# Kernel optimization log

Measured on AMD Instinct MI355X. Metric: run time of the kernel, lower is better.

## Reference

```python
import jax, jax.numpy as jnp
import numpy as np

N_NODES = 200000
IN_DIM = 128
HID = 64
WALK_LEN = 16          # max_step + 1
NUM_WALKS = 16         # = hidden_graphs, walks per graph
N_GRAPHS = 1024
PEN = 32
N_CLASSES = 10
BN_EPS = 1e-5


def setup_inputs() -> dict:
    key = jax.random.key(0)
    ks = jax.random.split(key, 16)
    x = jax.random.normal(ks[0], (N_NODES, IN_DIM), dtype=jnp.float32)
    walks = jax.random.randint(ks[1], (N_GRAPHS * NUM_WALKS, WALK_LEN), 0, N_NODES)
    # each graph contributes NUM_WALKS consecutive walks
    walk_batch = jnp.repeat(jnp.arange(N_GRAPHS), NUM_WALKS)
    s = 1.0 / np.sqrt(HID)
    return {
        "x": x,
        "walks": walks,
        "walk_batch": walk_batch,
        "W_enc": jax.random.normal(ks[2], (HID, IN_DIM), jnp.float32) / np.sqrt(IN_DIM),
        "b_enc": jnp.zeros((HID,), jnp.float32),
        "W_ih": jax.random.uniform(ks[3], (3 * HID, HID), jnp.float32, -s, s),
        "W_hh": jax.random.uniform(ks[4], (3 * HID, HID), jnp.float32, -s, s),
        "b_ih": jax.random.uniform(ks[5], (3 * HID,), jnp.float32, -s, s),
        "b_hh": jax.random.uniform(ks[6], (3 * HID,), jnp.float32, -s, s),
        "gamma": jnp.ones((HID,), jnp.float32),
        "beta": jnp.zeros((HID,), jnp.float32),
        "W1": jax.random.normal(ks[7], (PEN, HID), jnp.float32) / np.sqrt(HID),
        "b1": jnp.zeros((PEN,), jnp.float32),
        "W2": jax.random.normal(ks[8], (N_CLASSES, PEN), jnp.float32) / np.sqrt(PEN),
        "b2": jnp.zeros((N_CLASSES,), jnp.float32),
    }


def _gru_cell(h, xt, W_ih, W_hh, b_ih, b_hh):
    # PyTorch GRU gate math
    gi = xt @ W_ih.T + b_ih            # [W, 3H]
    gh = h @ W_hh.T + b_hh             # [W, 3H]
    i_r, i_z, i_n = jnp.split(gi, 3, axis=-1)
    h_r, h_z, h_n = jnp.split(gh, 3, axis=-1)
    r = jax.nn.sigmoid(i_r + h_r)
    z = jax.nn.sigmoid(i_z + h_z)
    n = jnp.tanh(i_n + r * h_n)
    return (1.0 - z) * n + z * h


def reference(x, walks, walk_batch, W_enc, b_enc, W_ih, W_hh, b_ih, b_hh,
              gamma, beta, W1, b1, W2, b2):
    # feature encoder on all nodes, then gather along walks
    x_enc = x @ W_enc.T + b_enc                     # [N, H]
    walk_feats = x_enc[walks]                       # [W, L, H] gather
    xs = jnp.swapaxes(walk_feats, 0, 1)             # [L, W, H]

    def step(h, xt):
        return _gru_cell(h, xt, W_ih, W_hh, b_ih, b_hh), None

    h0 = jnp.zeros((walks.shape[0], HID), walk_feats.dtype)
    h_final, _ = jax.lax.scan(step, h0, xs)         # [W, H] last hidden state

    # segment-mean pooling per graph
    seg_sum = jax.ops.segment_sum(h_final, walk_batch, num_segments=N_GRAPHS)
    cnt = jax.ops.segment_sum(jnp.ones((walks.shape[0],), h_final.dtype),
                              walk_batch, num_segments=N_GRAPHS)
    graph_enc = seg_sum / jnp.maximum(cnt, 1.0)[:, None]   # [B, H]

    # BatchNorm1d (training mode: batch statistics, biased variance)
    mean = jnp.mean(graph_enc, axis=0)
    var = jnp.mean(jnp.square(graph_enc - mean), axis=0)
    gn = (graph_enc - mean) / jnp.sqrt(var + BN_EPS) * gamma + beta

    h1 = jax.nn.relu(gn @ W1.T + b1)                # dropout p=0 -> identity
    logits = h1 @ W2.T + b2
    return jax.nn.log_softmax(logits, axis=1)
```

## Files before the change

### kernel.cpp

```cpp
#include <hip/hip_runtime.h>
#include <stdint.h>

typedef _Float16 half8 __attribute__((ext_vector_type(8)));
typedef _Float16 half4 __attribute__((ext_vector_type(4)));
typedef float f32x4 __attribute__((ext_vector_type(4)));

#define MFMA_F16(A, B, C) __builtin_amdgcn_mfma_f32_16x16x32_f16(A, B, C, 0, 0, 0)

#define NN 200000
#define NT 3125
#define GSTRIDE 512

__device__ __forceinline__ void gload_lds16(const void* gp, void* lp) {
  __builtin_amdgcn_global_load_lds(
      (const __attribute__((address_space(1))) uint32_t*)(gp),
      (__attribute__((address_space(3))) uint32_t*)(lp), 16, 0, 0);
}

__global__ __launch_bounds__(256, 2) void k_enc(const float* __restrict__ x,
                                                const float* __restrict__ Wenc,
                                                const float* __restrict__ benc,
                                                _Float16* __restrict__ xenc) {
  __shared__ float xl[2][64 * 128];
  __shared__ _Float16 wlds[16 * 64 * 8];

  const int tid = threadIdx.x;
  const int lane = tid & 63, wv = tid >> 6;
  const int r = lane & 15, g = lane >> 4;
  const int t0 = blockIdx.x;

#define ISSUE8(TT, BUF)                                                        \
  {                                                                            \
    _Pragma("unroll") for (int i = 0; i < 8; ++i) {                            \
      int row = wv * 16 + 2 * i + (lane >> 5);                                 \
      int grow = (TT) * 64 + row;                                              \
      if (grow >= NN) grow = NN - 1;                                           \
      int scol = ((lane & 31) * 16) ^ ((row & 7) << 4);                        \
      gload_lds16((const char*)(x + (size_t)grow * 128) + scol,                \
                  (char*)&xl[BUF][0] + (wv * 16 + 2 * i) * 512);               \
    }                                                                          \
  }

  ISSUE8(t0, 0);
  for (int i4 = tid; i4 < 2048; i4 += 256) {
    int idx = i4 * 4;
    f32x4 v = *(const f32x4*)(Wenc + idx);
    int j = idx >> 7, k = idx & 127;
    int tile = (j >> 4) * 4 + (k >> 5);
    int ln = ((k >> 3) & 3) * 16 + (j & 15);
    half4 h;
    h[0] = (_Float16)v[0]; h[1] = (_Float16)v[1];
    h[2] = (_Float16)v[2]; h[3] = (_Float16)v[3];
    *(half4*)&wlds[(tile * 64 + ln) * 8 + (k & 7)] = h;
  }
  __syncthreads();

  half8 W[4][4];
#pragma unroll
  for (int jt = 0; jt < 4; ++jt)
#pragma unroll
    for (int kt = 0; kt < 4; ++kt)
      W[jt][kt] = *(const half8*)&wlds[((jt * 4 + kt) * 64 + lane) * 8];

  float bb[4][4];
#pragma unroll
  for (int jt = 0; jt < 4; ++jt)
#pragma unroll
    for (int rr = 0; rr < 4; ++rr) bb[jt][rr] = benc[jt * 16 + g * 4 + rr];

  const int sw = (r & 7) << 4;
  int buf = 0;

  for (int t = t0; t < NT; t += GSTRIDE) {
    int tn = t + GSTRIDE;
    if (tn < NT) {
      ISSUE8(tn, buf ^ 1);
      asm volatile("s_waitcnt vmcnt(8)" ::: "memory");
    } else {
      asm volatile("s_waitcnt vmcnt(0)" ::: "memory");
    }
    __builtin_amdgcn_sched_barrier(0);

    const char* rp = (const char*)&xl[buf][0] + (wv * 16 + r) * 512;
    f32x4 acc[4];
#pragma unroll
    for (int jt = 0; jt < 4; ++jt)
      acc[jt] = (f32x4){bb[jt][0], bb[jt][1], bb[jt][2], bb[jt][3]};

#pragma unroll
    for (int kt = 0; kt < 4; ++kt) {
      f32x4 v0 = *(const f32x4*)(rp + ((kt * 128 + g * 32) ^ sw));
      f32x4 v1 = *(const f32x4*)(rp + ((kt * 128 + g * 32 + 16) ^ sw));
      half8 a;
#pragma unroll
      for (int e = 0; e < 4; ++e) {
        a[e] = (_Float16)v0[e];
        a[4 + e] = (_Float16)v1[e];
      }
#pragma unroll
      for (int jt = 0; jt < 4; ++jt)
        acc[jt] = MFMA_F16(W[jt][kt], a, acc[jt]);
    }

    int node = t * 64 + wv * 16 + r;
    if (node < NN) {
#pragma unroll
      for (int jt = 0; jt < 4; ++jt) {
        half4 o;
        o[0] = (_Float16)acc[jt][0]; o[1] = (_Float16)acc[jt][1];
        o[2] = (_Float16)acc[jt][2]; o[3] = (_Float16)acc[jt][3];
        *(half4*)&xenc[(size_t)node * 64 + jt * 16 + g * 4] = o;
      }
    }
    buf ^= 1;
  }
#undef ISSUE8
}

__global__ __launch_bounds__(512, 4) void k_gru(const _Float16* __restrict__ xenc,
                                                const int* __restrict__ walks,
                                                const float* __restrict__ Wih,
                                                const float* __restrict__ Whh,
                                                const float* __restrict__ bih,
                                                const float* __restrict__ bhh,
                                                float* __restrict__ genc) {
  __shared__ _Float16 wih_lds[24 * 64 * 8];
  __shared__ _Float16 whh_lds[24 * 64 * 8];
  __shared__ _Float16 h_lds[2][2][16 * 64];
  __shared__ int ids[2][256];

  const int tid = threadIdx.x;
  const int lane = tid & 63, wv = tid >> 6;
  const int r = lane & 15, g = lane >> 4;
  const int p = wv & 3;
  const int gl = wv >> 2;
  const int gph = blockIdx.x * 2 + gl;

  for (int idx = tid; idx < 192 * 64; idx += 512) {
    int j = idx >> 6, k = idx & 63;
    int tile = (j >> 4) * 2 + (k >> 5);
    int ln = ((k >> 3) & 3) * 16 + (j & 15);
    int off = (tile * 64 + ln) * 8 + (k & 7);
    wih_lds[off] = (_Float16)Wih[idx];
    whh_lds[off] = (_Float16)Whh[idx];
  }

  if ((wv & 3) == 0) {
    const int* wp = walks + gph * 256;
    int4 v = *(const int4*)(wp + lane * 4);
    int vals[4] = {v.x, v.y, v.z, v.w};
#pragma unroll
    for (int i = 0; i < 4; ++i) {
      int m = lane * 4 + i;
      ids[gl][(m & 15) * 16 + (m >> 4)] = vals[i];
    }
  }

  for (int i = tid; i < 4096; i += 512) ((_Float16*)h_lds)[i] = (_Float16)0.f;

  __syncthreads();

  half8 Bi[3][2], Bh[3][2];
#pragma unroll
  for (int G = 0; G < 3; ++G)
#pragma unroll
    for (int kt = 0; kt < 2; ++kt) {
      int T = G * 4 + p;
      Bi[G][kt] = *(const half8*)&wih_lds[((T * 2 + kt) * 64 + lane) * 8];
      Bh[G][kt] = *(const half8*)&whh_lds[((T * 2 + kt) * 64 + lane) * 8];
    }

  const int j0 = p * 16 + r;
  const float br_ = bih[j0] + bhh[j0];
  const float bz_ = bih[64 + j0] + bhh[64 + j0];
  const float bin_ = bih[128 + j0];
  const float bhn_ = bhh[128 + j0];

  f32x4 h = (f32x4){0.f, 0.f, 0.f, 0.f};
  const int swz = (r & 7) << 4;

  half8 AxA0, AxA1, AxB0, AxB1;
  {
    int n0 = ids[gl][0 * 16 + r];
    const _Float16* p0 = xenc + (size_t)n0 * 64 + g * 8;
    AxA0 = *(const half8*)p0;
    AxA1 = *(const half8*)(p0 + 32);
    int n1 = ids[gl][1 * 16 + r];
    const _Float16* p1 = xenc + (size_t)n1 * 64 + g * 8;
    AxB0 = *(const half8*)p1;
    AxB1 = *(const half8*)(p1 + 32);
  }

#define GRU_STEP(T_, RB, AX0, AX1)                                             \
  {                                                                            \
    int nid = ids[gl][(((T_) + 2) & 15) * 16 + r];                             \
    const _Float16* xp = xenc + (size_t)nid * 64 + g * 8;                      \
    half8 NX0 = *(const half8*)xp;                                             \
    half8 NX1 = *(const half8*)(xp + 32);                                      \
    char* rbase = (char*)&h_lds[gl][RB][0];                                    \
    char* wbase = (char*)&h_lds[gl][RB ^ 1][0];                                \
    half8 Ah0 = *(const half8*)(rbase + ((r * 128 + g * 16) ^ swz));           \
    half8 Ah1 = *(const half8*)(rbase + ((r * 128 + 64 + g * 16) ^ swz));      \
    f32x4 aR = (f32x4){br_, br_, br_, br_};                                    \
    f32x4 aZ = (f32x4){bz_, bz_, bz_, bz_};                                    \
    f32x4 aN = (f32x4){bin_, bin_, bin_, bin_};                                \
    f32x4 aH = (f32x4){bhn_, bhn_, bhn_, bhn_};                                \
    aR = MFMA_F16(AX0, Bi[0][0], aR);                                          \
    aR = MFMA_F16(AX1, Bi[0][1], aR);                                          \
    aZ = MFMA_F16(AX0, Bi[1][0], aZ);                                          \
    aZ = MFMA_F16(AX1, Bi[1][1], aZ);                                          \
    aN = MFMA_F16(AX0, Bi[2][0], aN);                                          \
    aN = MFMA_F16(AX1, Bi[2][1], aN);                                          \
    aR = MFMA_F16(Ah0, Bh[0][0], aR);                                          \
    aR = MFMA_F16(Ah1, Bh[0][1], aR);                                          \
    aZ = MFMA_F16(Ah0, Bh[1][0], aZ);                                          \
    aZ = MFMA_F16(Ah1, Bh[1][1], aZ);                                          \
    aH = MFMA_F16(Ah0, Bh[2][0], aH);                                          \
    aH = MFMA_F16(Ah1, Bh[2][1], aH);                                          \
    _Pragma("unroll") for (int rr = 0; rr < 4; ++rr) {                         \
      float rg = __builtin_amdgcn_rcpf(1.f + __expf(-aR[rr]));                 \
      float zg = __builtin_amdgcn_rcpf(1.f + __expf(-aZ[rr]));                 \
      float pn = aN[rr] + rg * aH[rr];                                         \
      float e2 = __expf(2.f * pn);                                             \
      float nn = 1.f - 2.f * __builtin_amdgcn_rcpf(e2 + 1.f);                  \
      h[rr] = (1.f - zg) * nn + zg * h[rr];                                    \
    }                                                                          \
    if ((T_) < 15) {                                                           \
      _Pragma("unroll") for (int rr = 0; rr < 4; ++rr) {                       \
        int row = g * 4 + rr;                                                  \
        int byte = (row * 128 + j0 * 2) ^ ((row & 7) << 4);                    \
        *(_Float16*)(wbase + byte) = (_Float16)h[rr];                          \
      }                                                                        \
    }                                                                          \
    asm volatile("s_waitcnt lgkmcnt(0)" ::: "memory");                         \
    __builtin_amdgcn_s_barrier();                                              \
    __builtin_amdgcn_sched_barrier(0);                                         \
    AX0 = NX0;                                                                 \
    AX1 = NX1;                                                                 \
  }

  for (int t = 0; t < 16; t += 2) {
    GRU_STEP(t, 0, AxA0, AxA1);
    GRU_STEP(t + 1, 1, AxB0, AxB1);
  }
#undef GRU_STEP

  {
    float s = h[0] + h[1] + h[2] + h[3];
    s += __shfl_xor(s, 16);
    s += __shfl_xor(s, 32);
    if (g == 0) genc[gph * 64 + j0] = s * 0.0625f;
  }
}

__global__ __launch_bounds__(256) void k_post(const float* __restrict__ genc,
                                              const float* __restrict__ gamma,
                                              const float* __restrict__ beta,
                                              const float* __restrict__ W1,
                                              const float* __restrict__ b1,
                                              const float* __restrict__ W2,
                                              const float* __restrict__ b2,
                                              float* __restrict__ out) {
  __shared__ float sum_s[4][64], sq_s[4][64], sc[64], sh[64];
  __shared__ float w1[32 * 64], w2[10 * 32], bb1[32], bb2[10];
  const int tid = threadIdx.x;
  const int j = tid & 63, grp = tid >> 6;

  float s = 0.f, q = 0.f;
  for (int rr = 0; rr < 256; ++rr) {
    float v = genc[(grp * 256 + rr) * 64 + j];
    s += v;
    q += v * v;
  }
  sum_s[grp][j] = s;
  sq_s[grp][j] = q;

  for (int i = tid; i < 32 * 64; i += 256) w1[i] = W1[i];
  for (int i = tid; i < 10 * 32; i += 256) w2[i] = W2[i];
  if (tid < 32) bb1[tid] = b1[tid];
  if (tid >= 32 && tid < 42) bb2[tid - 32] = b2[tid - 32];
  __syncthreads();

  if (grp == 0) {
    float S = sum_s[0][j] + sum_s[1][j] + sum_s[2][j] + sum_s[3][j];
    float Q = sq_s[0][j] + sq_s[1][j] + sq_s[2][j] + sq_s[3][j];
    float mean = S * (1.f / 1024.f);
    float var = Q * (1.f / 1024.f) - mean * mean;
    float rstd = rsqrtf(var + 1e-5f);
    float scv = gamma[j] * rstd;
    sc[j] = scv;
    sh[j] = beta[j] - mean * scv;
  }
  __syncthreads();

  const int row = blockIdx.x * 256 + tid;
  float gn[64];
  const f32x4* gp = (const f32x4*)(genc + row * 64);
#pragma unroll
  for (int jq = 0; jq < 16; ++jq) {
    f32x4 v = gp[jq];
#pragma unroll
    for (int e = 0; e < 4; ++e) gn[jq * 4 + e] = v[e] * sc[jq * 4 + e] + sh[jq * 4 + e];
  }

  float h1[32];
#pragma unroll
  for (int i = 0; i < 32; ++i) {
    float a = bb1[i];
#pragma unroll
    for (int jj = 0; jj < 64; ++jj) a += w1[i * 64 + jj] * gn[jj];
    h1[i] = fmaxf(a, 0.f);
  }

  float lg[10];
  float mx = -1e30f;
#pragma unroll
  for (int c = 0; c < 10; ++c) {
    float a = bb2[c];
#pragma unroll
    for (int i = 0; i < 32; ++i) a += w2[c * 32 + i] * h1[i];
    lg[c] = a;
    mx = fmaxf(mx, a);
  }
  float se = 0.f;
#pragma unroll
  for (int c = 0; c < 10; ++c) se += __expf(lg[c] - mx);
  float lse = mx + __logf(se);
#pragma unroll
  for (int c = 0; c < 10; ++c) out[row * 10 + c] = lg[c] - lse;
}

extern "C" void kernel_launch(void* const* d_in, const int* in_sizes, int n_in,
                              void* d_out, int out_size, void* d_ws, size_t ws_size,
                              hipStream_t stream) {
  const float* x = (const float*)d_in[0];
  const int* walks = (const int*)d_in[1];
  const float* Wenc = (const float*)d_in[3];
  const float* benc = (const float*)d_in[4];
  const float* Wih = (const float*)d_in[5];
  const float* Whh = (const float*)d_in[6];
  const float* bih = (const float*)d_in[7];
  const float* bhh = (const float*)d_in[8];
  const float* gamma = (const float*)d_in[9];
  const float* beta = (const float*)d_in[10];
  const float* W1 = (const float*)d_in[11];
  const float* b1 = (const float*)d_in[12];
  const float* W2 = (const float*)d_in[13];
  const float* b2 = (const float*)d_in[14];
  float* out = (float*)d_out;

  char* ws = (char*)d_ws;
  _Float16* xenc = (_Float16*)ws;
  float* genc = (float*)(ws + 25600000);

  k_enc<<<dim3(GSTRIDE), dim3(256), 0, stream>>>(x, Wenc, benc, xenc);
  k_gru<<<dim3(512), dim3(512), 0, stream>>>(xenc, walks, Wih, Whh, bih, bhh, genc);
  k_post<<<dim3(4), dim3(256), 0, stream>>>(genc, gamma, beta, W1, b1, W2, b2, out);
}
```

Before: 81.64 us.

## Fold encoder into GRU input weights and gather raw node features per walk

Drops the full-graph encoder pass. A small prep kernel precomputes W_ih·W_enc (and the combined bias), so the GRU kernel gathers raw 128-dim fp32 rows of x only for the walked nodes. It converts them to fp16 and stages them in LDS with double buffering. This avoids encoding all 200k nodes and writing/reading the intermediate, and only 262k gathered rows are touched. In exchange the GRU does twice the input-gate MFMAs and gathers larger fp32 rows on its critical path.

```diff
diff --git a/kernel.cpp b/kernel.cpp
--- a/kernel.cpp
+++ b/kernel.cpp
@@ -2,147 +2,89 @@
 #include <stdint.h>
 
 typedef _Float16 half8 __attribute__((ext_vector_type(8)));
-typedef _Float16 half4 __attribute__((ext_vector_type(4)));
 typedef float f32x4 __attribute__((ext_vector_type(4)));
 
 #define MFMA_F16(A, B, C) __builtin_amdgcn_mfma_f32_16x16x32_f16(A, B, C, 0, 0, 0)
 
-#define NN 200000
-#define NT 3125
-#define GSTRIDE 512
-
-__device__ __forceinline__ void gload_lds16(const void* gp, void* lp) {
-  __builtin_amdgcn_global_load_lds(
-      (const __attribute__((address_space(1))) uint32_t*)(gp),
-      (__attribute__((address_space(3))) uint32_t*)(lp), 16, 0, 0);
+
+__global__ __launch_bounds__(256) void k_prep(const float* __restrict__ Wenc,
+                                              const float* __restrict__ benc,
+                                              const float* __restrict__ Wih,
+                                              const float* __restrict__ Whh,
+                                              const float* __restrict__ bih,
+                                              _Float16* __restrict__ wgi,
+                                              _Float16* __restrict__ whhp,
+                                              float* __restrict__ bc) {
+  __shared__ float wenc_s[64 * 68];
+  __shared__ float wih_s[16 * 64];
+  const int t = threadIdx.x;
+  const int bt = blockIdx.x;
+  const int jt = bt >> 1, kh = (bt & 1) << 6;
+
+  for (int i = t; i < 4096; i += 256)
+    wenc_s[(i >> 6) * 68 + (i & 63)] = Wenc[(i >> 6) * 128 + kh + (i & 63)];
+  for (int i = t; i < 1024; i += 256)
+    wih_s[i] = Wih[(jt * 16 + (i >> 6)) * 64 + (i & 63)];
+  __syncthreads();
+
+  const int jl = t >> 4, kb = (t & 15) * 4;
+  f32x4 acc = (f32x4){0.f, 0.f, 0.f, 0.f};
+  for (int m = 0; m < 64; ++m) {
+    float w = wih_s[jl * 64 + m];
+    f32x4 v = *(const f32x4*)&wenc_s[m * 68 + kb];
+    acc[0] += w * v[0]; acc[1] += w * v[1];
+    acc[2] += w * v[2]; acc[3] += w * v[3];
+  }
+#pragma unroll
+  for (int i = 0; i < 4; ++i) {
+    int k = kh + kb + i;
+    wgi[((jt * 4 + (k >> 5)) * 64 + ((k >> 3) & 3) * 16 + jl) * 8 + (k & 7)] =
+        (_Float16)acc[i];
+  }
+
+  if ((bt & 1) == 0) {
+#pragma unroll
+    for (int i = 0; i < 4; ++i) {
+      int idx = t * 4 + i;
+      int j = jt * 16 + (idx >> 6), k = idx & 63;
+      whhp[((jt * 2 + (k >> 5)) * 64 + ((k >> 3) & 3) * 16 + (j & 15)) * 8 + (k & 7)] =
+          (_Float16)Whh[j * 64 + k];
+    }
+    if (t < 16) {
+      int j = jt * 16 + t;
+      float s = bih[j];
+      for (int m = 0; m < 64; ++m) s += wih_s[t * 64 + m] * benc[m];
+      bc[j] = s;
+    }
+  }
 }
 
-__global__ __launch_bounds__(256, 2) void k_enc(const float* __restrict__ x,
-                                                const float* __restrict__ Wenc,
-                                                const float* __restrict__ benc,
-                                                _Float16* __restrict__ xenc) {
-  __shared__ float xl[2][64 * 128];
-  __shared__ _Float16 wlds[16 * 64 * 8];
+__global__ __launch_bounds__(512, 4) void k_gru(const float* __restrict__ x,
+                                                const int* __restrict__ walks,
+                                                const _Float16* __restrict__ wgi,
+                                                const _Float16* __restrict__ whhp,
+                                                const float* __restrict__ bc,
+                                                const float* __restrict__ bhh,
+                                                float* __restrict__ genc) {
+  __shared__ _Float16 xs[2][2][2048];
+  __shared__ _Float16 h_lds[2][2][1024];
+  __shared__ int ids[2][256];
 
   const int tid = threadIdx.x;
   const int lane = tid & 63, wv = tid >> 6;
   const int r = lane & 15, g = lane >> 4;
-  const int t0 = blockIdx.x;
-
-#define ISSUE8(TT, BUF)                                                        \
-  {                                                                            \
-    _Pragma("unroll") for (int i = 0; i < 8; ++i) {                            \
-      int row = wv * 16 + 2 * i + (lane >> 5);                                 \
-      int grow = (TT) * 64 + row;                                              \
-      if (grow >= NN) grow = NN - 1;                                           \
-      int scol = ((lane & 31) * 16) ^ ((row & 7) << 4);                        \
-      gload_lds16((const char*)(x + (size_t)grow * 128) + scol,                \
-                  (char*)&xl[BUF][0] + (wv * 16 + 2 * i) * 512);               \
-    }                                                                          \
-  }
-
-  ISSUE8(t0, 0);
-  for (int i4 = tid; i4 < 2048; i4 += 256) {
-    int idx = i4 * 4;
-    f32x4 v = *(const f32x4*)(Wenc + idx);
-    int j = idx >> 7, k = idx & 127;
-    int tile = (j >> 4) * 4 + (k >> 5);
-    int ln = ((k >> 3) & 3) * 16 + (j & 15);
-    half4 h;
-    h[0] = (_Float16)v[0]; h[1] = (_Float16)v[1];
-    h[2] = (_Float16)v[2]; h[3] = (_Float16)v[3];
-    *(half4*)&wlds[(tile * 64 + ln) * 8 + (k & 7)] = h;
-  }
-  __syncthreads();
-
-  half8 W[4][4];
-#pragma unroll
-  for (int jt = 0; jt < 4; ++jt)
+  const int p = wv & 3, gl = wv >> 2;
+  const int gph = blockIdx.x * 2 + gl;
+
+  half8 Bi[3][4], Bh[3][2];
+#pragma unroll
+  for (int G = 0; G < 3; ++G) {
 #pragma unroll
     for (int kt = 0; kt < 4; ++kt)
-      W[jt][kt] = *(const half8*)&wlds[((jt * 4 + kt) * 64 + lane) * 8];
-
-  float bb[4][4];
-#pragma unroll
-  for (int jt = 0; jt < 4; ++jt)
-#pragma unroll
-    for (int rr = 0; rr < 4; ++rr) bb[jt][rr] = benc[jt * 16 + g * 4 + rr];
-
-  const int sw = (r & 7) << 4;
-  int buf = 0;
-
-  for (int t = t0; t < NT; t += GSTRIDE) {
-    int tn = t + GSTRIDE;
-    if (tn < NT) {
-      ISSUE8(tn, buf ^ 1);
-      asm volatile("s_waitcnt vmcnt(8)" ::: "memory");
-    } else {
-      asm volatile("s_waitcnt vmcnt(0)" ::: "memory");
-    }
-    __builtin_amdgcn_sched_barrier(0);
-
-    const char* rp = (const char*)&xl[buf][0] + (wv * 16 + r) * 512;
-    f32x4 acc[4];
-#pragma unroll
-    for (int jt = 0; jt < 4; ++jt)
-      acc[jt] = (f32x4){bb[jt][0], bb[jt][1], bb[jt][2], bb[jt][3]};
-
-#pragma unroll
-    for (int kt = 0; kt < 4; ++kt) {
-      f32x4 v0 = *(const f32x4*)(rp + ((kt * 128 + g * 32) ^ sw));
-      f32x4 v1 = *(const f32x4*)(rp + ((kt * 128 + g * 32 + 16) ^ sw));
-      half8 a;
-#pragma unroll
-      for (int e = 0; e < 4; ++e) {
-        a[e] = (_Float16)v0[e];
-        a[4 + e] = (_Float16)v1[e];
-      }
-#pragma unroll
-      for (int jt = 0; jt < 4; ++jt)
-        acc[jt] = MFMA_F16(W[jt][kt], a, acc[jt]);
-    }
-
-    int node = t * 64 + wv * 16 + r;
-    if (node < NN) {
-#pragma unroll
-      for (int jt = 0; jt < 4; ++jt) {
-        half4 o;
-        o[0] = (_Float16)acc[jt][0]; o[1] = (_Float16)acc[jt][1];
-        o[2] = (_Float16)acc[jt][2]; o[3] = (_Float16)acc[jt][3];
-        *(half4*)&xenc[(size_t)node * 64 + jt * 16 + g * 4] = o;
-      }
-    }
-    buf ^= 1;
-  }
-#undef ISSUE8
-}
-
-__global__ __launch_bounds__(512, 4) void k_gru(const _Float16* __restrict__ xenc,
-                                                const int* __restrict__ walks,
-                                                const float* __restrict__ Wih,
-                                                const float* __restrict__ Whh,
-                                                const float* __restrict__ bih,
-                                                const float* __restrict__ bhh,
-                                                float* __restrict__ genc) {
-  __shared__ _Float16 wih_lds[24 * 64 * 8];
-  __shared__ _Float16 whh_lds[24 * 64 * 8];
-  __shared__ _Float16 h_lds[2][2][16 * 64];
-  __shared__ int ids[2][256];
-
-  const int tid = threadIdx.x;
-  const int lane = tid & 63, wv = tid >> 6;
-  const int r = lane & 15, g = lane >> 4;
-  const int p = wv & 3;
-  const int gl = wv >> 2;
-  const int gph = blockIdx.x * 2 + gl;
-
-  for (int idx = tid; idx < 192 * 64; idx += 512) {
-    int j = idx >> 6, k = idx & 63;
-    int tile = (j >> 4) * 2 + (k >> 5);
-    int ln = ((k >> 3) & 3) * 16 + (j & 15);
-    int off = (tile * 64 + ln) * 8 + (k & 7);
-    wih_lds[off] = (_Float16)Wih[idx];
-    whh_lds[off] = (_Float16)Whh[idx];
+      Bi[G][kt] = *(const half8*)&wgi[(((G * 4 + p) * 4 + kt) * 64 + lane) * 8];
+#pragma unroll
+    for (int kt = 0; kt < 2; ++kt)
+      Bh[G][kt] = *(const half8*)&whhp[(((G * 4 + p) * 2 + kt) * 64 + lane) * 8];
   }
 
   if ((wv & 3) == 0) {
@@ -155,62 +97,70 @@
       ids[gl][(m & 15) * 16 + (m >> 4)] = vals[i];
     }
   }
-
   for (int i = tid; i < 4096; i += 512) ((_Float16*)h_lds)[i] = (_Float16)0.f;
-
-  __syncthreads();
-
-  half8 Bi[3][2], Bh[3][2];
-#pragma unroll
-  for (int G = 0; G < 3; ++G)
-#pragma unroll
-    for (int kt = 0; kt < 2; ++kt) {
-      int T = G * 4 + p;
-      Bi[G][kt] = *(const half8*)&wih_lds[((T * 2 + kt) * 64 + lane) * 8];
-      Bh[G][kt] = *(const half8*)&whh_lds[((T * 2 + kt) * 64 + lane) * 8];
+  __syncthreads();
+
+  const int j0 = p * 16 + r;
+  const float br_ = bc[j0] + bhh[j0];
+  const float bz_ = bc[64 + j0] + bhh[64 + j0];
+  const float bin_ = bc[128 + j0];
+  const float bhn_ = bhh[128 + j0];
+  const int swz = (r & 7) << 4;
+
+  char* xg = (char*)&xs[gl][0][0];
+  char* hg = (char*)&h_lds[gl][0][0];
+  const int xwb = r * 256 + ((p * 64 + g * 16) ^ swz);
+
+#pragma unroll
+  for (int tt = 0; tt < 2; ++tt) {
+    int nid = ids[gl][tt * 16 + r];
+    const f32x4* px = (const f32x4*)(x + (size_t)nid * 128 + p * 32 + g * 8);
+    f32x4 a = px[0], b = px[1];
+    half8 hx;
+#pragma unroll
+    for (int e = 0; e < 4; ++e) {
+      hx[e] = (_Float16)a[e];
+      hx[4 + e] = (_Float16)b[e];
     }
-
-  const int j0 = p * 16 + r;
-  const float br_ = bih[j0] + bhh[j0];
-  const float bz_ = bih[64 + j0] + bhh[64 + j0];
-  const float bin_ = bih[128 + j0];
-  const float bhn_ = bhh[128 + j0];
-
+    *(half8*)(xg + tt * 4096 + xwb) = hx;
+  }
   f32x4 h = (f32x4){0.f, 0.f, 0.f, 0.f};
-  const int swz = (r & 7) << 4;
-
-  half8 AxA0, AxA1, AxB0, AxB1;
-  {
-    int n0 = ids[gl][0 * 16 + r];
-    const _Float16* p0 = xenc + (size_t)n0 * 64 + g * 8;
-    AxA0 = *(const half8*)p0;
-    AxA1 = *(const half8*)(p0 + 32);
-    int n1 = ids[gl][1 * 16 + r];
-    const _Float16* p1 = xenc + (size_t)n1 * 64 + g * 8;
-    AxB0 = *(const half8*)p1;
-    AxB1 = *(const half8*)(p1 + 32);
-  }
-
-#define GRU_STEP(T_, RB, AX0, AX1)                                             \
+  __syncthreads();
+
+  f32x4 eP0, eP1, oP0, oP1;
+
+#define GRU_STEP(T_, ISS0, ISS1, CV0, CV1)                                     \
   {                                                                            \
-    int nid = ids[gl][(((T_) + 2) & 15) * 16 + r];                             \
-    const _Float16* xp = xenc + (size_t)nid * 64 + g * 8;                      \
-    half8 NX0 = *(const half8*)xp;                                             \
-    half8 NX1 = *(const half8*)(xp + 32);                                      \
-    char* rbase = (char*)&h_lds[gl][RB][0];                                    \
-    char* wbase = (char*)&h_lds[gl][RB ^ 1][0];                                \
-    half8 Ah0 = *(const half8*)(rbase + ((r * 128 + g * 16) ^ swz));           \
-    half8 Ah1 = *(const half8*)(rbase + ((r * 128 + 64 + g * 16) ^ swz));      \
+    int nid2 = ids[gl][(((T_) + 2) & 15) * 16 + r];                            \
+    const f32x4* px = (const f32x4*)(x + (size_t)nid2 * 128 + p * 32 + g * 8); \
+    ISS0 = px[0];                                                              \
+    ISS1 = px[1];                                                              \
+    const int RB = (T_) & 1;                                                   \
+    char* xb = xg + RB * 4096;                                                 \
+    char* rbh = hg + RB * 2048;                                                \
+    char* wbh = hg + (RB ^ 1) * 2048;                                          \
+    half8 Ax0 = *(const half8*)(xb + r * 256 + ((g * 16) ^ swz));              \
+    half8 Ax1 = *(const half8*)(xb + r * 256 + ((64 + g * 16) ^ swz));         \
+    half8 Ax2 = *(const half8*)(xb + r * 256 + ((128 + g * 16) ^ swz));        \
+    half8 Ax3 = *(const half8*)(xb + r * 256 + ((192 + g * 16) ^ swz));        \
+    half8 Ah0 = *(const half8*)(rbh + ((r * 128 + g * 16) ^ swz));             \
+    half8 Ah1 = *(const half8*)(rbh + ((r * 128 + 64 + g * 16) ^ swz));        \
     f32x4 aR = (f32x4){br_, br_, br_, br_};                                    \
     f32x4 aZ = (f32x4){bz_, bz_, bz_, bz_};                                    \
     f32x4 aN = (f32x4){bin_, bin_, bin_, bin_};                                \
     f32x4 aH = (f32x4){bhn_, bhn_, bhn_, bhn_};                                \
-    aR = MFMA_F16(AX0, Bi[0][0], aR);                                          \
-    aR = MFMA_F16(AX1, Bi[0][1], aR);                                          \
-    aZ = MFMA_F16(AX0, Bi[1][0], aZ);                                          \
-    aZ = MFMA_F16(AX1, Bi[1][1], aZ);                                          \
-    aN = MFMA_F16(AX0, Bi[2][0], aN);                                          \
-    aN = MFMA_F16(AX1, Bi[2][1], aN);                                          \
+    aR = MFMA_F16(Ax0, Bi[0][0], aR);                                          \
+    aR = MFMA_F16(Ax1, Bi[0][1], aR);                                          \
+    aR = MFMA_F16(Ax2, Bi[0][2], aR);                                          \
+    aR = MFMA_F16(Ax3, Bi[0][3], aR);                                          \
+    aZ = MFMA_F16(Ax0, Bi[1][0], aZ);                                          \
+    aZ = MFMA_F16(Ax1, Bi[1][1], aZ);                                          \
+    aZ = MFMA_F16(Ax2, Bi[1][2], aZ);                                          \
+    aZ = MFMA_F16(Ax3, Bi[1][3], aZ);                                          \
+    aN = MFMA_F16(Ax0, Bi[2][0], aN);                                          \
+    aN = MFMA_F16(Ax1, Bi[2][1], aN);                                          \
+    aN = MFMA_F16(Ax2, Bi[2][2], aN);                                          \
+    aN = MFMA_F16(Ax3, Bi[2][3], aN);                                          \
     aR = MFMA_F16(Ah0, Bh[0][0], aR);                                          \
     aR = MFMA_F16(Ah1, Bh[0][1], aR);                                          \
     aZ = MFMA_F16(Ah0, Bh[1][0], aZ);                                          \
@@ -229,19 +179,25 @@
       _Pragma("unroll") for (int rr = 0; rr < 4; ++rr) {                       \
         int row = g * 4 + rr;                                                  \
         int byte = (row * 128 + j0 * 2) ^ ((row & 7) << 4);                    \
-        *(_Float16*)(wbase + byte) = (_Float16)h[rr];                          \
+        *(_Float16*)(wbh + byte) = (_Float16)h[rr];                            \
       }                                                                        \
+    }                                                                          \
+    if ((T_) >= 1 && (T_) < 15) {    \
+      half8 hx;                                                                \
+      _Pragma("unroll") for (int e = 0; e < 4; ++e) {                          \
+        hx[e] = (_Float16)CV0[e];                                              \
+        hx[4 + e] = (_Float16)CV1[e];                                          \
+      }                                                                        \
+      *(half8*)(xg + (((T_) + 1) & 1) * 4096 + xwb) = hx;                      \
     }                                                                          \
     asm volatile("s_waitcnt lgkmcnt(0)" ::: "memory");                         \
     __builtin_amdgcn_s_barrier();                                              \
     __builtin_amdgcn_sched_barrier(0);                                         \
-    AX0 = NX0;                                                                 \
-    AX1 = NX1;                                                                 \
   }
 
   for (int t = 0; t < 16; t += 2) {
-    GRU_STEP(t, 0, AxA0, AxA1);
-    GRU_STEP(t + 1, 1, AxB0, AxB1);
+    GRU_STEP(t, eP0, eP1, oP0, oP1);
+    GRU_STEP(t + 1, oP0, oP1, eP0, eP1);
   }
 #undef GRU_STEP
 
@@ -350,10 +306,12 @@
   float* out = (float*)d_out;
 
   char* ws = (char*)d_ws;
-  _Float16* xenc = (_Float16*)ws;
-  float* genc = (float*)(ws + 25600000);
-
-  k_enc<<<dim3(GSTRIDE), dim3(256), 0, stream>>>(x, Wenc, benc, xenc);
-  k_gru<<<dim3(512), dim3(512), 0, stream>>>(xenc, walks, Wih, Whh, bih, bhh, genc);
+  _Float16* wgi = (_Float16*)ws;
+  _Float16* whhp = (_Float16*)(ws + 49152);
+  float* bcb = (float*)(ws + 73728);
+  float* genc = (float*)(ws + 74752);
+
+  k_prep<<<dim3(24), dim3(256), 0, stream>>>(Wenc, benc, Wih, Whh, bih, wgi, whhp, bcb);
+  k_gru<<<dim3(512), dim3(512), 0, stream>>>(x, walks, wgi, whhp, bcb, bhh, genc);
   k_post<<<dim3(4), dim3(256), 0, stream>>>(genc, gamma, beta, W1, b1, W2, b2, out);
 }
```

Result: slower. 141.3 us (+73.1%).
